# Kernel optimization log

Measured on AMD Instinct MI355X. Metric: run time of the kernel, lower is better.

The kernel has to match this reference:

```python
import jax, jax.numpy as jnp
import numpy as np

N_EMBD = 2048
EXPAND = 2
D_INNER = N_EMBD * EXPAND          # 4096
D_STATE = 128
N_HEADS = D_INNER // D_STATE       # 32
HEAD_DIM = D_INNER // N_HEADS      # 128
N_GROUPS = 1
D_CONV = 4
CHUNK = 64
N_LAYERS = 48
GS = N_GROUPS * D_STATE
PROJ = 2 * D_INNER + N_HEADS + 2 * GS  # 8480
RMS_EPS = 1e-6


def _ssd_scan(A, B, C, dt, x, chunk_size=CHUNK):
    """Mamba-2 SSD chunked selective scan. A:(b,t,h) B,C:(b,t,g,n) dt:(b,t,h) x:(b,t,h,p)."""
    batch, seq_len, n_heads, P = x.shape
    G, N = B.shape[2], B.shape[3]
    Hg = n_heads // G
    Q = chunk_size
    pad_len = -seq_len % Q
    if pad_len:
        A = jnp.pad(A, ((0, 0), (0, pad_len), (0, 0)))
        B = jnp.pad(B, ((0, 0), (0, pad_len), (0, 0), (0, 0)))
        C = jnp.pad(C, ((0, 0), (0, pad_len), (0, 0), (0, 0)))
        dt = jnp.pad(dt, ((0, 0), (0, pad_len), (0, 0)))
        x = jnp.pad(x, ((0, 0), (0, pad_len), (0, 0), (0, 0)))
    T_pad = seq_len + pad_len
    n_chunks = T_pad // Q
    A_c = A.reshape(batch, n_chunks, Q, n_heads)
    B_c = B.reshape(batch, n_chunks, Q, G, N)
    C_c = C.reshape(batch, n_chunks, Q, G, N)
    dt_c = dt.reshape(batch, n_chunks, Q, n_heads)
    x_c = x.reshape(batch, n_chunks, Q, n_heads, P)
    log_a = A_c * dt_c
    cum_log_a = jnp.cumsum(log_a, axis=2)
    chunk_log_decay = cum_log_a[:, :, -1, :]
    log_diff = cum_log_a[:, :, :, None, :] - cum_log_a[:, :, None, :, :]
    causal = jnp.tril(jnp.ones((Q, Q), dtype=jnp.bool_))[None, None, :, :, None]
    L = jnp.exp(jnp.where(causal, log_diff, -jnp.inf))
    CB = jnp.einsum('bcign,bcjgn->bcijg', C_c, B_c)
    L_rs = L.reshape(batch, n_chunks, Q, Q, G, Hg)
    dt_rs = dt_c.reshape(batch, n_chunks, Q, G, Hg)
    x_rs = x_c.reshape(batch, n_chunks, Q, G, Hg, P)
    y_intra = jnp.einsum('bcijGH,bcijG,bcjGH,bcjGHp->bciGHp', L_rs, CB, dt_rs, x_rs)
    decay_to_end = jnp.exp(chunk_log_decay[:, :, None, :] - cum_log_a)
    decay_to_end_rs = decay_to_end.reshape(batch, n_chunks, Q, G, Hg)
    state_local = jnp.einsum('bcjGH,bcjGH,bcjGn,bcjGHp->bcGHnp', decay_to_end_rs, dt_rs, B_c, x_rs)
    chunk_decay = jnp.exp(chunk_log_decay).reshape(batch, n_chunks, G, Hg)

    def scan_op(left, right):
        d_l, s_l = left
        d_r, s_r = right
        return (d_l * d_r, d_r[..., None, None] * s_l + s_r)

    _, state_at_end = jax.lax.associative_scan(scan_op, (chunk_decay, state_local), axis=1)
    state_at_start = jnp.concatenate([jnp.zeros_like(state_at_end[:, :1]), state_at_end[:, :-1]], axis=1)
    decay_from_start = jnp.exp(cum_log_a).reshape(batch, n_chunks, Q, G, Hg)
    y_inter = jnp.einsum('bciGH,bciGn,bcGHnp->bciGHp', decay_from_start, C_c, state_at_start)
    y = (y_intra + y_inter).reshape(batch, T_pad, n_heads, P)
    if pad_len:
        y = y[:, :seq_len]
    return y


def setup_inputs() -> dict:
    key = jax.random.key(0)
    ks = jax.random.split(key, 6)
    Bsz, T = 2, 2048
    x = jax.random.normal(ks[0], (Bsz, T, N_EMBD), jnp.float32)
    norm_scale = jnp.ones((N_EMBD,), jnp.float32)
    in_proj_w = 0.02 * jax.random.normal(ks[1], (N_EMBD, PROJ), jnp.float32)
    conv_weight = 0.02 * jax.random.normal(ks[2], (D_CONV, D_INNER), jnp.float32)
    conv_bias = jnp.zeros((D_INNER,), jnp.float32)
    A_log = jnp.log(jnp.arange(1, N_HEADS + 1, dtype=jnp.float32))
    dt_bias = 0.1 * jax.random.normal(ks[3], (N_HEADS,), jnp.float32)
    D = jnp.ones((D_INNER,), jnp.float32)
    out_proj_w = (0.02 / np.sqrt(2 * N_LAYERS)) * jax.random.normal(ks[4], (D_INNER, N_EMBD), jnp.float32)
    return dict(x=x, norm_scale=norm_scale, in_proj_w=in_proj_w, conv_weight=conv_weight,
                conv_bias=conv_bias, A_log=A_log, dt_bias=dt_bias, D=D, out_proj_w=out_proj_w)


def reference(x, norm_scale, in_proj_w, conv_weight, conv_bias, A_log, dt_bias, D, out_proj_w):
    residual = x
    b, t = x.shape[0], x.shape[1]
    # RMSNorm
    h = x * jax.lax.rsqrt(jnp.mean(x * x, axis=-1, keepdims=True) + RMS_EPS) * norm_scale
    proj = h @ in_proj_w  # (b, t, PROJ)
    gate = proj[..., :D_INNER]
    ssm_in = proj[..., D_INNER:2 * D_INNER]
    dt_raw = proj[..., 2 * D_INNER:2 * D_INNER + N_HEADS]
    Bm = proj[..., 2 * D_INNER + N_HEADS:2 * D_INNER + N_HEADS + GS].reshape(b, t, N_GROUPS, D_STATE)
    Cm = proj[..., 2 * D_INNER + N_HEADS + GS:].reshape(b, t, N_GROUPS, D_STATE)
    # causal depthwise short conv
    xp = jnp.pad(ssm_in, ((0, 0), (D_CONV - 1, 0), (0, 0)))
    w_t = conv_weight.T[:, None, :]  # (D_INNER, 1, D_CONV)
    y = jax.lax.conv_general_dilated(jnp.transpose(xp, (0, 2, 1)), w_t,
                                     window_strides=(1,), padding='VALID',
                                     feature_group_count=D_INNER)
    ssm_in = jnp.transpose(y, (0, 2, 1)) + conv_bias
    ssm_in = jax.nn.silu(ssm_in)
    dt = jax.nn.softplus(dt_raw + dt_bias)
    A = -jnp.exp(A_log)
    A_f = jnp.broadcast_to(A[None, None, :], (b, t, N_HEADS))
    x_h = ssm_in.reshape(b, t, N_HEADS, HEAD_DIM)
    y_ssd = _ssd_scan(A_f, Bm, Cm, dt, x_h).reshape(b, t, D_INNER)
    y_ssd = y_ssd + D * ssm_in
    y_ssd = y_ssd * jax.nn.silu(gate)
    return residual + y_ssd @ out_proj_w
```

## Files before the change

kernel.cpp:

```cpp
#include <hip/hip_runtime.h>

typedef unsigned short u16;
typedef unsigned short u16x8 __attribute__((ext_vector_type(8)));
typedef __bf16 bf16x8 __attribute__((ext_vector_type(8)));
typedef float f32x4 __attribute__((ext_vector_type(4)));


__device__ __forceinline__ float bf2f(u16 u) {
    union { unsigned int i; float f; } v; v.i = ((unsigned int)u) << 16; return v.f;
}
__device__ __forceinline__ u16 f2bf(float f) {
    unsigned int u = __float_as_uint(f);
    u += 0x7fffu + ((u >> 16) & 1u);
    return (u16)(u >> 16);
}
__device__ __forceinline__ bf16x8 ld8(const u16* p) {
    return __builtin_bit_cast(bf16x8, *reinterpret_cast<const u16x8*>(p));
}
__device__ __forceinline__ void load_lds16(const u16* g, u16* l) {
    __builtin_amdgcn_global_load_lds(
        (const __attribute__((address_space(1))) unsigned int*)g,
        (__attribute__((address_space(3))) unsigned int*)l, 16, 0, 0);
}
__device__ __forceinline__ float fexp(float x) { return __expf(x); }
__device__ __forceinline__ float frcp(float x) { return __builtin_amdgcn_rcpf(x); }

__global__ __launch_bounds__(256) void k_rmsnorm(const float* __restrict__ x,
                                                 const float* __restrict__ scale,
                                                 u16* __restrict__ h) {
    int row = blockIdx.x, tid = threadIdx.x;
    const float4* xr = reinterpret_cast<const float4*>(x + (size_t)row * 2048);
    float4 v0 = xr[tid], v1 = xr[tid + 256];
    float ss = v0.x*v0.x + v0.y*v0.y + v0.z*v0.z + v0.w*v0.w
             + v1.x*v1.x + v1.y*v1.y + v1.z*v1.z + v1.w*v1.w;
#pragma unroll
    for (int off = 32; off > 0; off >>= 1) ss += __shfl_down(ss, off, 64);
    __shared__ float red[4];
    if ((tid & 63) == 0) red[tid >> 6] = ss;
    __syncthreads();
    float r = rsqrtf((red[0] + red[1] + red[2] + red[3]) * (1.f / 2048.f) + 1e-6f);
    const float4* sc = reinterpret_cast<const float4*>(scale);
    float4 s0 = sc[tid], s1 = sc[tid + 256];
    ushort4 o0, o1;
    o0.x = f2bf(v0.x * r * s0.x); o0.y = f2bf(v0.y * r * s0.y);
    o0.z = f2bf(v0.z * r * s0.z); o0.w = f2bf(v0.w * r * s0.w);
    o1.x = f2bf(v1.x * r * s1.x); o1.y = f2bf(v1.y * r * s1.y);
    o1.z = f2bf(v1.z * r * s1.z); o1.w = f2bf(v1.w * r * s1.w);
    ushort4* hr = reinterpret_cast<ushort4*>(h + (size_t)row * 2048);
    hr[tid] = o0; hr[tid + 256] = o1;
}

__global__ __launch_bounds__(256) void k_wcast(const float* __restrict__ W,
                                               u16* __restrict__ Wt,
                                               int K, int N) {
    __shared__ u16 Ts[64][72];
    int n0 = blockIdx.x * 64, k0 = blockIdx.y * 64;
    int t = threadIdx.x;
    int jl = (t & 15) * 4;
#pragma unroll
    for (int s = 0; s < 4; ++s) {
        int kl = s * 16 + (t >> 4);
        if (n0 + jl + 4 <= N) {
            float4 v = *reinterpret_cast<const float4*>(W + (size_t)(k0 + kl) * N + n0 + jl);
            Ts[kl][jl] = f2bf(v.x); Ts[kl][jl + 1] = f2bf(v.y);
            Ts[kl][jl + 2] = f2bf(v.z); Ts[kl][jl + 3] = f2bf(v.w);
        } else {
#pragma unroll
            for (int e = 0; e < 4; ++e)
                Ts[kl][jl + e] = (n0 + jl + e < N) ? f2bf(W[(size_t)(k0 + kl) * N + n0 + jl + e]) : (u16)0;
        }
    }
    __syncthreads();
    int nl = t >> 2, kl0 = (t & 3) * 16;
    u16 tmp[16];
#pragma unroll
    for (int e = 0; e < 16; ++e) tmp[e] = Ts[kl0 + e][nl];
    u16* dst = Wt + (size_t)(n0 + nl) * K + k0 + kl0;
    *reinterpret_cast<uint4*>(dst) = *reinterpret_cast<uint4*>(tmp);
    *reinterpret_cast<uint4*>(dst + 8) = *reinterpret_cast<uint4*>(tmp + 8);
}

template <bool BF16_OUT, int MAP>
__global__ __launch_bounds__(256) void k_gemm128(const u16* __restrict__ A,
                                                 const u16* __restrict__ Bt,
                                                 u16* __restrict__ Cb,
                                                 float* __restrict__ Cf,
                                                 const float* __restrict__ resid,
                                                 int M, int Nw, int ldc, int ncoff,
                                                 int K, int nbt) {
    __shared__ u16 As[8192];
    __shared__ u16 Bs[8192];
    int bid = blockIdx.x;
    int mb, nb;
    if (MAP == 0) {
        int mt = M >> 7;
        int grp = mt * 8;
        int g = bid / grp, l = bid % grp;
        nb = g * 8 + (l & 7); mb = l >> 3;
        if (nb * 128 >= Nw) return;
    } else {
        nb = bid % nbt; mb = bid / nbt;
    }
    int m0 = mb * 128, n0 = nb * 128;

    int t = threadIdx.x, lane = t & 63, w = t >> 6;
    int row = t >> 2, kc = (t & 3) * 8;
    int wm = (w >> 1) * 64, wn = (w & 1) * 64;
    int r = lane & 15, q = lane >> 4;

    f32x4 acc[4][4];
#pragma unroll
    for (int a = 0; a < 4; ++a)
#pragma unroll
        for (int b = 0; b < 4; ++b) acc[a][b] = (f32x4){0.f, 0.f, 0.f, 0.f};

    const u16* ga0 = A + (size_t)(m0 + row) * K + kc;
    const u16* ga1 = A + (size_t)(m0 + 64 + row) * K + kc;
    const u16* gb0 = Bt + (size_t)(ncoff + n0 + row) * K + kc;
    const u16* gb1 = Bt + (size_t)(ncoff + n0 + 64 + row) * K + kc;

    for (int k0 = 0; k0 < K; k0 += 64) {
        load_lds16(ga0 + k0,      As + w * 512);
        load_lds16(ga1 + k0,      As + 2048 + w * 512);
        load_lds16(gb0 + k0,      Bs + w * 512);
        load_lds16(gb1 + k0,      Bs + 2048 + w * 512);
        load_lds16(ga0 + k0 + 32, As + 4096 + w * 512);
        load_lds16(ga1 + k0 + 32, As + 4096 + 2048 + w * 512);
        load_lds16(gb0 + k0 + 32, Bs + 4096 + w * 512);
        load_lds16(gb1 + k0 + 32, Bs + 4096 + 2048 + w * 512);
        __syncthreads();
#pragma unroll
        for (int h = 0; h < 2; ++h) {
            bf16x8 af[4], bf[4];
#pragma unroll
            for (int mi = 0; mi < 4; ++mi) af[mi] = ld8(&As[h * 4096 + (wm + mi * 16 + r) * 32 + q * 8]);
#pragma unroll
            for (int ni = 0; ni < 4; ++ni) bf[ni] = ld8(&Bs[h * 4096 + (wn + ni * 16 + r) * 32 + q * 8]);
#pragma unroll
            for (int mi = 0; mi < 4; ++mi)
#pragma unroll
                for (int ni = 0; ni < 4; ++ni)
                    acc[mi][ni] = __builtin_amdgcn_mfma_f32_16x16x32_bf16(af[mi], bf[ni], acc[mi][ni], 0, 0, 0);
        }
        __syncthreads();
    }
#pragma unroll
    for (int mi = 0; mi < 4; ++mi)
#pragma unroll
        for (int ni = 0; ni < 4; ++ni) {
            int lgn = n0 + wn + ni * 16 + r;
            if (lgn < Nw) {
#pragma unroll
                for (int rg = 0; rg < 4; ++rg) {
                    int gm = m0 + wm + mi * 16 + q * 4 + rg;
                    float vv = acc[mi][ni][rg];
                    if (BF16_OUT) {
                        Cb[(size_t)gm * ldc + ncoff + lgn] = f2bf(vv);
                    } else {
                        if (resid) vv += resid[(size_t)gm * ldc + ncoff + lgn];
                        Cf[(size_t)gm * ldc + ncoff + lgn] = vv;
                    }
                }
            }
        }
}

template <bool F32OUT>
__global__ __launch_bounds__(512, 2) void k_gemm256(const u16* __restrict__ A,
                                                    const u16* __restrict__ Bt,
                                                    u16* __restrict__ Cb,
                                                    float* __restrict__ Cf,
                                                    int M, int Nout, int ldc,
                                                    int lda, int Kl) {
    __shared__ u16 lds[65536];
    const int nkt = Kl >> 6;
    int mt = M >> 8;
    int bid = blockIdx.x;
    int swz = (bid & 7) * ((int)gridDim.x >> 3) + (bid >> 3);
    int tiles = mt * (Nout >> 8);
    int tp = swz % tiles, ks = swz / tiles;
    int mb = tp % mt, nb = tp / mt;
    int m0 = mb << 8, n0 = nb << 8;
    int koff = ks * Kl;

    int t = threadIdx.x;
    int ln = t & 63, w = t >> 6;
    int wm = w >> 2, wn = w & 3;
    int r = ln & 15, q = ln >> 4;
    int xq = (q << 3) ^ ((r & 7) << 3);

    int rr = ln >> 3;
    int cc8 = ((ln & 7) ^ rr) << 3;
    const u16* Ag = A + (size_t)(m0 + w * 8 + rr) * lda + koff + cc8;
    const u16* Bg = Bt + (size_t)(n0 + w * 8 + rr) * lda + koff + cc8;
    u16* ldsw = lds + (w << 9);
    const size_t R64 = (size_t)lda * 64;
    const size_t R128 = (size_t)lda * 128;

    f32x4 acc[8][4];
#pragma unroll
    for (int a = 0; a < 8; ++a)
#pragma unroll
        for (int b = 0; b < 4; ++b) acc[a][b] = (f32x4){0.f, 0.f, 0.f, 0.f};

    auto stageA = [&](int ti, int h) {
        if (ti >= nkt) return;
        const u16* g = Ag + ((size_t)ti << 6) + (h ? R128 : (size_t)0);
        u16* d = ldsw + ((ti & 1) << 14) + (h << 13);
        load_lds16(g, d);
        load_lds16(g + R64, d + 4096);
    };
    auto stageB = [&](int ti, int h) {
        if (ti >= nkt) return;
        const u16* g = Bg + ((size_t)ti << 6) + (h ? R128 : (size_t)0);
        u16* d = ldsw + 32768 + ((ti & 1) << 14) + (h << 13);
        load_lds16(g, d);
        load_lds16(g + R64, d + 4096);
    };

    stageA(0, 0); stageA(0, 1); stageB(0, 0); stageB(0, 1);
    stageA(1, 0); stageA(1, 1); stageB(1, 0); stageB(1, 1);
    asm volatile("s_waitcnt vmcnt(8)" ::: "memory");
    __builtin_amdgcn_s_barrier();
    asm volatile("" ::: "memory");

    bf16x8 aF[4][2], bLo[2][2], bHi[2][2];

    for (int kt = 0; kt < nkt; ++kt) {
        const u16* Ah = lds + ((kt & 1) << 14) + (wm << 13);
        const u16* Bh = lds + 32768 + ((kt & 1) << 14) + ((wn >> 1) << 13) + ((wn & 1) << 12);

#pragma unroll
        for (int mi = 0; mi < 4; ++mi)
#pragma unroll
            for (int ks2 = 0; ks2 < 2; ++ks2)
                aF[mi][ks2] = ld8(Ah + (mi * 16 + r) * 64 + (xq ^ (ks2 << 5)));
#pragma unroll
        for (int ni = 0; ni < 2; ++ni)
#pragma unroll
            for (int ks2 = 0; ks2 < 2; ++ks2)
                bLo[ni][ks2] = ld8(Bh + (ni * 16 + r) * 64 + (xq ^ (ks2 << 5)));
        asm volatile("" ::: "memory");
        __builtin_amdgcn_s_barrier();
        asm volatile("s_waitcnt lgkmcnt(0)" ::: "memory");
        __builtin_amdgcn_s_setprio(1);
#pragma unroll
        for (int mi = 0; mi < 4; ++mi)
#pragma unroll
            for (int ni = 0; ni < 2; ++ni)
#pragma unroll
                for (int ks2 = 0; ks2 < 2; ++ks2)
                    acc[mi][ni] = __builtin_amdgcn_mfma_f32_16x16x32_bf16(aF[mi][ks2], bLo[ni][ks2], acc[mi][ni], 0, 0, 0);
        __builtin_amdgcn_s_setprio(0);
        asm volatile("" ::: "memory");
        __builtin_amdgcn_s_barrier();
        asm volatile("" ::: "memory");

#pragma unroll
        for (int ni = 0; ni < 2; ++ni)
#pragma unroll
            for (int ks2 = 0; ks2 < 2; ++ks2)
                bHi[ni][ks2] = ld8(Bh + ((ni + 2) * 16 + r) * 64 + (xq ^ (ks2 << 5)));
        asm volatile("" ::: "memory");
        __builtin_amdgcn_s_barrier();
        asm volatile("s_waitcnt lgkmcnt(0)" ::: "memory");
        __builtin_amdgcn_s_setprio(1);
#pragma unroll
        for (int mi = 0; mi < 4; ++mi)
#pragma unroll
            for (int ni = 0; ni < 2; ++ni)
#pragma unroll
                for (int ks2 = 0; ks2 < 2; ++ks2)
                    acc[mi][ni + 2] = __builtin_amdgcn_mfma_f32_16x16x32_bf16(aF[mi][ks2], bHi[ni][ks2], acc[mi][ni + 2], 0, 0, 0);
        __builtin_amdgcn_s_setprio(0);
        asm volatile("" ::: "memory");
        __builtin_amdgcn_s_barrier();
        asm volatile("" ::: "memory");

#pragma unroll
        for (int mi = 0; mi < 4; ++mi)
#pragma unroll
            for (int ks2 = 0; ks2 < 2; ++ks2)
                aF[mi][ks2] = ld8(Ah + ((mi + 4) * 16 + r) * 64 + (xq ^ (ks2 << 5)));
        stageB(kt + 2, 0);
        stageB(kt + 2, 1);
        asm volatile("" ::: "memory");
        __builtin_amdgcn_s_barrier();
        asm volatile("s_waitcnt lgkmcnt(0)" ::: "memory");
        __builtin_amdgcn_s_setprio(1);
#pragma unroll
        for (int mi = 0; mi < 4; ++mi)
#pragma unroll
            for (int ni = 0; ni < 2; ++ni)
#pragma unroll
                for (int ks2 = 0; ks2 < 2; ++ks2)
                    acc[mi + 4][ni + 2] = __builtin_amdgcn_mfma_f32_16x16x32_bf16(aF[mi][ks2], bHi[ni][ks2], acc[mi + 4][ni + 2], 0, 0, 0);
        __builtin_amdgcn_s_setprio(0);
        asm volatile("" ::: "memory");
        __builtin_amdgcn_s_barrier();
        asm volatile("" ::: "memory");

        stageA(kt + 2, 0);
        stageA(kt + 2, 1);
        __builtin_amdgcn_s_setprio(1);
#pragma unroll
        for (int mi = 0; mi < 4; ++mi)
#pragma unroll
            for (int ni = 0; ni < 2; ++ni)
#pragma unroll
                for (int ks2 = 0; ks2 < 2; ++ks2)
                    acc[mi + 4][ni] = __builtin_amdgcn_mfma_f32_16x16x32_bf16(aF[mi][ks2], bLo[ni][ks2], acc[mi + 4][ni], 0, 0, 0);
        __builtin_amdgcn_s_setprio(0);
        if (kt + 2 < nkt) { asm volatile("s_waitcnt vmcnt(8)" ::: "memory"); }
        else              { asm volatile("s_waitcnt vmcnt(0)" ::: "memory"); }
        __builtin_amdgcn_s_barrier();
        asm volatile("" ::: "memory");
    }

#pragma unroll
    for (int mi = 0; mi < 8; ++mi)
#pragma unroll
        for (int ni = 0; ni < 4; ++ni) {
            int gn = n0 + wn * 64 + ni * 16 + r;
            if (gn < Nout) {
#pragma unroll
                for (int rg = 0; rg < 4; ++rg) {
                    int gm = m0 + wm * 128 + mi * 16 + q * 4 + rg;
                    if (F32OUT) {
                        Cf[(size_t)ks * M * Nout + (size_t)gm * Nout + gn] = acc[mi][ni][rg];
                    } else {
                        Cb[(size_t)gm * ldc + gn] = f2bf(acc[mi][ni][rg]);
                    }
                }
            }
        }
}

__global__ __launch_bounds__(256) void k_addred(const float* __restrict__ x,
                                                const float* __restrict__ P0,
                                                const float* __restrict__ P1,
                                                float* __restrict__ out) {
    const float4* xv = reinterpret_cast<const float4*>(x);
    const float4* a = reinterpret_cast<const float4*>(P0);
    const float4* b = reinterpret_cast<const float4*>(P1);
    float4* o = reinterpret_cast<float4*>(out);
    for (int k = blockIdx.x * 256 + threadIdx.x; k < 2097152; k += 524288) {
        float4 xx = xv[k], aa = a[k], bb = b[k];
        float4 r;
        r.x = xx.x + aa.x + bb.x; r.y = xx.y + aa.y + bb.y;
        r.z = xx.z + aa.z + bb.z; r.w = xx.w + aa.w + bb.w;
        o[k] = r;
    }
}

__global__ __launch_bounds__(64) void k_dt(const u16* __restrict__ proj,
                                           const float* __restrict__ A_log,
                                           const float* __restrict__ dt_bias,
                                           float* __restrict__ dt,
                                           float* __restrict__ cumla) {
    int bid = blockIdx.x;
    int b = bid >> 10, hh = (bid >> 5) & 31, c = bid & 31;
    int j = threadIdx.x;
    int t = c * 64 + j;
    float z = bf2f(proj[(size_t)(b * 2048 + t) * 8480 + 8192 + hh]) + dt_bias[hh];
    float dtv = (z > 20.f) ? z : log1pf(fexp(z));
    float v = -fexp(A_log[hh]) * dtv;
#pragma unroll
    for (int off = 1; off < 64; off <<= 1) {
        float pv = __shfl_up(v, off, 64);
        if (j >= off) v += pv;
    }
    int base = ((b * 32 + hh) * 32 + c) * 64;
    dt[base + j] = dtv;
    cumla[base + j] = v;
}

__global__ __launch_bounds__(256) void k_intra(const u16* __restrict__ proj,
                                               const float* __restrict__ dt,
                                               const float* __restrict__ cumla,
                                               const float* __restrict__ cw,
                                               const float* __restrict__ cb,
                                               const float* __restrict__ Dv,
                                               u16* __restrict__ ybuf,
                                               u16* __restrict__ states) {
    __shared__ u16 Xt[128][72];
    __shared__ u16 Bt[128][72];
    __shared__ union {
        u16 Ms[64][72];
        struct { float cwl[4][128]; float cbl[128]; } cv;
    } sh;
    __shared__ float dts[64], clas[64];
    int bid = blockIdx.x;
    int b = bid >> 10, c = (bid >> 5) & 31, hh = bid & 31;
    int tid = threadIdx.x, lane = tid & 63, w = tid >> 6;
    int r = lane & 15, q = lane >> 4;
    int t0 = b * 2048 + c * 64;
    int sbase = ((b * 32 + hh) * 32 + c) * 64;

    if (tid < 64) { dts[tid] = dt[sbase + tid]; clas[tid] = cumla[sbase + tid]; }
    if (tid < 128) {
        sh.cv.cbl[tid] = cb[hh * 128 + tid];
#pragma unroll
        for (int k = 0; k < 4; ++k) sh.cv.cwl[k][tid] = cw[k * 4096 + hh * 128 + tid];
    }
    __syncthreads();

    {
        int j = tid & 63;
        float wj = fexp(clas[63] - clas[j]) * dts[j];
        for (int g = tid >> 6; g < 16; g += 4) {
            int p0 = g * 8;
            u16 tb[8];
            *reinterpret_cast<uint4*>(tb) =
                *reinterpret_cast<const uint4*>(proj + (size_t)(t0 + j) * 8480 + 8224 + p0);
            float xv[8];
#pragma unroll
            for (int e = 0; e < 8; ++e) xv[e] = sh.cv.cbl[p0 + e];
#pragma unroll
            for (int kk = 0; kk < 4; ++kk) {
                int tl = c * 64 + j - 3 + kk;
                if (tl >= 0) {
                    u16 srow[8];
                    *reinterpret_cast<uint4*>(srow) =
                        *reinterpret_cast<const uint4*>(proj + (size_t)(b * 2048 + tl) * 8480 + 4096 + hh * 128 + p0);
#pragma unroll
                    for (int e = 0; e < 8; ++e) xv[e] += sh.cv.cwl[kk][p0 + e] * bf2f(srow[e]);
                }
            }
#pragma unroll
            for (int e = 0; e < 8; ++e) {
                float s = xv[e] * frcp(1.f + fexp(-xv[e]));
                Xt[p0 + e][j] = f2bf(s);
                Bt[p0 + e][j] = f2bf(wj * bf2f(tb[e]));
            }
        }
    }
    __syncthreads();

    {
        const u16* crow = proj + (size_t)(t0 + w * 16 + r) * 8480 + 8352;
        bf16x8 af[4];
#pragma unroll
        for (int k = 0; k < 4; ++k) af[k] = ld8(crow + k * 32 + q * 8);
#pragma unroll
        for (int tj = 0; tj < 4; ++tj) {
            const u16* brow = proj + (size_t)(t0 + tj * 16 + r) * 8480 + 8224;
            f32x4 acc = (f32x4){0.f, 0.f, 0.f, 0.f};
#pragma unroll
            for (int k = 0; k < 4; ++k)
                acc = __builtin_amdgcn_mfma_f32_16x16x32_bf16(af[k], ld8(brow + k * 32 + q * 8), acc, 0, 0, 0);
            int j = tj * 16 + r;
            float dj = dts[j], cj = clas[j];
#pragma unroll
            for (int rg = 0; rg < 4; ++rg) {
                int i = w * 16 + q * 4 + rg;
                float m = (j <= i) ? acc[rg] * fexp(clas[i] - cj) * dj : 0.f;
                sh.Ms[i][j] = f2bf(m);
            }
        }
    }
    __syncthreads();

    {
        bf16x8 af[2];
#pragma unroll
        for (int k = 0; k < 2; ++k) af[k] = ld8(&sh.Ms[w * 16 + r][k * 32 + q * 8]);
#pragma unroll
        for (int tj = 0; tj < 8; ++tj) {
            f32x4 acc = (f32x4){0.f, 0.f, 0.f, 0.f};
#pragma unroll
            for (int k = 0; k < 2; ++k)
                acc = __builtin_amdgcn_mfma_f32_16x16x32_bf16(af[k], ld8(&Xt[tj * 16 + r][k * 32 + q * 8]), acc, 0, 0, 0);
            int p = tj * 16 + r;
            float dv = Dv[hh * 128 + p];
#pragma unroll
            for (int rg = 0; rg < 4; ++rg) {
                int i = w * 16 + q * 4 + rg;
                float v = acc[rg] + dv * bf2f(Xt[p][i]);
                ybuf[(size_t)(t0 + i) * 4096 + hh * 128 + p] = f2bf(v);
            }
        }
    }

    size_t sb = ((size_t)((b * 32 + hh) * 32 + c)) * 16384;
#pragma unroll
    for (int th = 0; th < 2; ++th) {
        int ti = w + th * 4;
        bf16x8 af[2];
#pragma unroll
        for (int k = 0; k < 2; ++k) af[k] = ld8(&Xt[ti * 16 + r][k * 32 + q * 8]);
#pragma unroll
        for (int tj = 0; tj < 8; ++tj) {
            f32x4 acc = (f32x4){0.f, 0.f, 0.f, 0.f};
#pragma unroll
            for (int k = 0; k < 2; ++k)
                acc = __builtin_amdgcn_mfma_f32_16x16x32_bf16(af[k], ld8(&Bt[tj * 16 + r][k * 32 + q * 8]), acc, 0, 0, 0);
            int n = tj * 16 + r;
#pragma unroll
            for (int rg = 0; rg < 4; ++rg) {
                int p = ti * 16 + q * 4 + rg;
                states[sb + p * 128 + n] = f2bf(acc[rg]);
            }
        }
    }
}

__global__ __launch_bounds__(256) void k_scan(u16* __restrict__ states,
                                              const float* __restrict__ cumla) {
    int gid = blockIdx.x * 256 + threadIdx.x;
    int bh = gid >> 12;
    int q4 = (gid & 4095) * 4;
    size_t base = (size_t)bh * 32 * 16384 + q4;
    float s0 = 0.f, s1 = 0.f, s2 = 0.f, s3 = 0.f;
    for (int c = 0; c < 32; ++c) {
        float cd = fexp(cumla[(bh * 32 + c) * 64 + 63]);
        size_t idx = base + (size_t)c * 16384;
        ushort4 v = *reinterpret_cast<ushort4*>(states + idx);
        float l0 = bf2f(v.x), l1 = bf2f(v.y), l2 = bf2f(v.z), l3 = bf2f(v.w);
        ushort4 o; o.x = f2bf(s0); o.y = f2bf(s1); o.z = f2bf(s2); o.w = f2bf(s3);
        *reinterpret_cast<ushort4*>(states + idx) = o;
        s0 = cd * s0 + l0; s1 = cd * s1 + l1; s2 = cd * s2 + l2; s3 = cd * s3 + l3;
    }
}

__global__ __launch_bounds__(256) void k_inter(const u16* __restrict__ proj,
                                               const u16* __restrict__ states,
                                               const float* __restrict__ cumla,
                                               const u16* __restrict__ ybuf,
                                               u16* __restrict__ ygated) {
    __shared__ u16 Ss[128][136];
    __shared__ float clav[64];
    int bid = blockIdx.x;
    int b = bid >> 10, c = (bid >> 5) & 31, hh = bid & 31;
    int tid = threadIdx.x, lane = tid & 63, w = tid >> 6;
    int r = lane & 15, q = lane >> 4;
    int t0 = b * 2048 + c * 64;
    int sbase = ((b * 32 + hh) * 32 + c) * 64;
    size_t sb = ((size_t)((b * 32 + hh) * 32 + c)) * 16384;

    if (tid < 64) clav[tid] = fexp(cumla[sbase + tid]);
    for (int e = tid; e < 2048; e += 256) {
        int p = e >> 4, n8 = (e & 15) * 8;
        *reinterpret_cast<uint4*>(&Ss[p][n8]) =
            *reinterpret_cast<const uint4*>(states + sb + p * 128 + n8);
    }
    __syncthreads();

    const u16* crow = proj + (size_t)(t0 + w * 16 + r) * 8480 + 8352;
    bf16x8 af[4];
#pragma unroll
    for (int k = 0; k < 4; ++k) af[k] = ld8(crow + k * 32 + q * 8);
#pragma unroll
    for (int tj = 0; tj < 8; ++tj) {
        f32x4 acc = (f32x4){0.f, 0.f, 0.f, 0.f};
#pragma unroll
        for (int k = 0; k < 4; ++k)
            acc = __builtin_amdgcn_mfma_f32_16x16x32_bf16(af[k], ld8(&Ss[tj * 16 + r][k * 32 + q * 8]), acc, 0, 0, 0);
        int p = tj * 16 + r;
        int ch = hh * 128 + p;
#pragma unroll
        for (int rg = 0; rg < 4; ++rg) {
            int i = w * 16 + q * 4 + rg;
            size_t td = (size_t)(t0 + i) * 4096 + ch;
            float v = clav[i] * acc[rg] + bf2f(ybuf[td]);
            float g = bf2f(proj[(size_t)(t0 + i) * 8480 + ch]);
            ygated[td] = f2bf(v * (g * frcp(1.f + fexp(-g))));
        }
    }
}

extern "C" void kernel_launch(void* const* d_in, const int* in_sizes, int n_in,
                              void* d_out, int out_size, void* d_ws, size_t ws_size,
                              hipStream_t stream) {
    const float* x          = (const float*)d_in[0];
    const float* norm_scale = (const float*)d_in[1];
    const float* in_proj_w  = (const float*)d_in[2];
    const float* conv_w     = (const float*)d_in[3];
    const float* conv_b     = (const float*)d_in[4];
    const float* A_log      = (const float*)d_in[5];
    const float* dt_bias    = (const float*)d_in[6];
    const float* Dv         = (const float*)d_in[7];
    const float* out_w      = (const float*)d_in[8];
    float* out = (float*)d_out;

    char* ws = (char*)d_ws;
    u16*   states = (u16*)(ws);
    u16*   h      = (u16*)(ws);
    u16*   wbt    = (u16*)(ws + 16777216);
    float* parts  = (float*)(ws);
    u16*   proj   = (u16*)(ws + 67108864);
    u16*   owt    = (u16*)(ws + 136577024);
    u16*   ybuf   = (u16*)(ws + 170131456);
    float* dt     = (float*)(ws + 203685888);
    float* cumla  = (float*)(ws + 204210176);

    k_rmsnorm<<<4096, 256, 0, stream>>>(x, norm_scale, h);
    k_wcast<<<dim3(136, 32), 256, 0, stream>>>(in_proj_w, wbt, 2048, 8480);
    k_gemm128<true, 1><<<96, 256, 0, stream>>>(h, wbt, proj, nullptr, nullptr,
                                               4096, 288, 8480, 8192, 2048, 3);
    k_gemm256<false><<<512, 512, 0, stream>>>(h, wbt, proj, nullptr,
                                              4096, 8192, 8480, 2048, 2048);
    k_dt<<<2048, 64, 0, stream>>>(proj, A_log, dt_bias, dt, cumla);
    k_intra<<<2048, 256, 0, stream>>>(proj, dt, cumla, conv_w, conv_b, Dv, ybuf, states);
    k_scan<<<1024, 256, 0, stream>>>(states, cumla);
    k_inter<<<2048, 256, 0, stream>>>(proj, states, cumla, ybuf, ybuf);
    k_wcast<<<dim3(32, 64), 256, 0, stream>>>(out_w, owt, 4096, 2048);
    k_gemm256<true><<<256, 512, 0, stream>>>(ybuf, owt, nullptr, parts,
                                             4096, 2048, 2048, 4096, 2048);
    k_addred<<<2048, 256, 0, stream>>>(x, parts, parts + 8388608, out);
}
```

Baseline: 548.0 us.

## Split-K the projection tail GEMM and restagger gemm256 prefetch issue

```diff
diff --git a/kernel.cpp b/kernel.cpp
--- a/kernel.cpp
+++ b/kernel.cpp
@@ -80,28 +80,20 @@
     *reinterpret_cast<uint4*>(dst + 8) = *reinterpret_cast<uint4*>(tmp + 8);
 }
 
-template <bool BF16_OUT, int MAP>
-__global__ __launch_bounds__(256) void k_gemm128(const u16* __restrict__ A,
-                                                 const u16* __restrict__ Bt,
-                                                 u16* __restrict__ Cb,
-                                                 float* __restrict__ Cf,
-                                                 const float* __restrict__ resid,
-                                                 int M, int Nw, int ldc, int ncoff,
-                                                 int K, int nbt) {
+template <int SPLITK>
+__global__ __launch_bounds__(256) void k_tail(const u16* __restrict__ A,
+                                              const u16* __restrict__ Bt,
+                                              float* __restrict__ Pf,
+                                              int M, int ncoff, int lda, int nbt) {
     __shared__ u16 As[8192];
     __shared__ u16 Bs[8192];
+    const int Ks = lda / SPLITK;
     int bid = blockIdx.x;
-    int mb, nb;
-    if (MAP == 0) {
-        int mt = M >> 7;
-        int grp = mt * 8;
-        int g = bid / grp, l = bid % grp;
-        nb = g * 8 + (l & 7); mb = l >> 3;
-        if (nb * 128 >= Nw) return;
-    } else {
-        nb = bid % nbt; mb = bid / nbt;
-    }
+    int nb = bid % nbt;
+    int ksl = (bid / nbt) % SPLITK;
+    int mb = bid / (nbt * SPLITK);
     int m0 = mb * 128, n0 = nb * 128;
+    int koff = ksl * Ks;
 
     int t = threadIdx.x, lane = t & 63, w = t >> 6;
     int row = t >> 2, kc = (t & 3) * 8;
@@ -114,12 +106,12 @@
 #pragma unroll
         for (int b = 0; b < 4; ++b) acc[a][b] = (f32x4){0.f, 0.f, 0.f, 0.f};
 
-    const u16* ga0 = A + (size_t)(m0 + row) * K + kc;
-    const u16* ga1 = A + (size_t)(m0 + 64 + row) * K + kc;
-    const u16* gb0 = Bt + (size_t)(ncoff + n0 + row) * K + kc;
-    const u16* gb1 = Bt + (size_t)(ncoff + n0 + 64 + row) * K + kc;
-
-    for (int k0 = 0; k0 < K; k0 += 64) {
+    const u16* ga0 = A + (size_t)(m0 + row) * lda + koff + kc;
+    const u16* ga1 = A + (size_t)(m0 + 64 + row) * lda + koff + kc;
+    const u16* gb0 = Bt + (size_t)(ncoff + n0 + row) * lda + koff + kc;
+    const u16* gb1 = Bt + (size_t)(ncoff + n0 + 64 + row) * lda + koff + kc;
+
+    for (int k0 = 0; k0 < Ks; k0 += 64) {
         load_lds16(ga0 + k0,      As + w * 512);
         load_lds16(ga1 + k0,      As + 2048 + w * 512);
         load_lds16(gb0 + k0,      Bs + w * 512);
@@ -149,20 +141,27 @@
 #pragma unroll
         for (int ni = 0; ni < 4; ++ni) {
             int lgn = n0 + wn + ni * 16 + r;
-            if (lgn < Nw) {
-#pragma unroll
-                for (int rg = 0; rg < 4; ++rg) {
-                    int gm = m0 + wm + mi * 16 + q * 4 + rg;
-                    float vv = acc[mi][ni][rg];
-                    if (BF16_OUT) {
-                        Cb[(size_t)gm * ldc + ncoff + lgn] = f2bf(vv);
-                    } else {
-                        if (resid) vv += resid[(size_t)gm * ldc + ncoff + lgn];
-                        Cf[(size_t)gm * ldc + ncoff + lgn] = vv;
-                    }
-                }
+#pragma unroll
+            for (int rg = 0; rg < 4; ++rg) {
+                int gm = m0 + wm + mi * 16 + q * 4 + rg;
+                Pf[((size_t)ksl * M + gm) * 384 + lgn] = acc[mi][ni][rg];
             }
         }
+}
+
+__global__ __launch_bounds__(256) void k_tailred(const float* __restrict__ Pf,
+                                                 u16* __restrict__ proj) {
+    int gid = blockIdx.x * 256 + threadIdx.x;
+    int rowi = gid / 72, c4 = (gid % 72) * 4;
+    const float4* P = reinterpret_cast<const float4*>(Pf);
+    int idx = rowi * 96 + (c4 >> 2);
+    float4 s0 = P[idx], s1 = P[393216 + idx], s2 = P[786432 + idx], s3 = P[1179648 + idx];
+    ushort4 o;
+    o.x = f2bf(s0.x + s1.x + s2.x + s3.x);
+    o.y = f2bf(s0.y + s1.y + s2.y + s3.y);
+    o.z = f2bf(s0.z + s1.z + s2.z + s3.z);
+    o.w = f2bf(s0.w + s1.w + s2.w + s3.w);
+    *reinterpret_cast<ushort4*>(proj + (size_t)rowi * 8480 + 8192 + c4) = o;
 }
 
 template <bool F32OUT>
@@ -218,9 +217,9 @@
         load_lds16(g + R64, d + 4096);
     };
 
-    stageA(0, 0); stageA(0, 1); stageB(0, 0); stageB(0, 1);
-    stageA(1, 0); stageA(1, 1); stageB(1, 0); stageB(1, 1);
-    asm volatile("s_waitcnt vmcnt(8)" ::: "memory");
+    stageA(0, 0); stageB(0, 0); stageB(0, 1); stageA(0, 1);
+    stageA(1, 0); stageB(1, 0); stageB(1, 1);
+    asm volatile("s_waitcnt vmcnt(6)" ::: "memory");
     __builtin_amdgcn_s_barrier();
     asm volatile("" ::: "memory");
 
@@ -240,6 +239,7 @@
 #pragma unroll
             for (int ks2 = 0; ks2 < 2; ++ks2)
                 bLo[ni][ks2] = ld8(Bh + (ni * 16 + r) * 64 + (xq ^ (ks2 << 5)));
+        stageA(kt + 1, 1);
         asm volatile("" ::: "memory");
         __builtin_amdgcn_s_barrier();
         asm volatile("s_waitcnt lgkmcnt(0)" ::: "memory");
@@ -283,7 +283,6 @@
             for (int ks2 = 0; ks2 < 2; ++ks2)
                 aF[mi][ks2] = ld8(Ah + ((mi + 4) * 16 + r) * 64 + (xq ^ (ks2 << 5)));
         stageB(kt + 2, 0);
-        stageB(kt + 2, 1);
         asm volatile("" ::: "memory");
         __builtin_amdgcn_s_barrier();
         asm volatile("s_waitcnt lgkmcnt(0)" ::: "memory");
@@ -300,8 +299,10 @@
         __builtin_amdgcn_s_barrier();
         asm volatile("" ::: "memory");
 
+        stageB(kt + 2, 1);
         stageA(kt + 2, 0);
-        stageA(kt + 2, 1);
+        asm volatile("" ::: "memory");
+        __builtin_amdgcn_s_barrier();
         __builtin_amdgcn_s_setprio(1);
 #pragma unroll
         for (int mi = 0; mi < 4; ++mi)
@@ -311,7 +312,7 @@
                 for (int ks2 = 0; ks2 < 2; ++ks2)
                     acc[mi + 4][ni] = __builtin_amdgcn_mfma_f32_16x16x32_bf16(aF[mi][ks2], bLo[ni][ks2], acc[mi + 4][ni], 0, 0, 0);
         __builtin_amdgcn_s_setprio(0);
-        if (kt + 2 < nkt) { asm volatile("s_waitcnt vmcnt(8)" ::: "memory"); }
+        if (kt + 2 < nkt) { asm volatile("s_waitcnt vmcnt(6)" ::: "memory"); }
         else              { asm volatile("s_waitcnt vmcnt(0)" ::: "memory"); }
         __builtin_amdgcn_s_barrier();
         asm volatile("" ::: "memory");
@@ -591,13 +592,14 @@
     u16*   proj   = (u16*)(ws + 67108864);
     u16*   owt    = (u16*)(ws + 136577024);
     u16*   ybuf   = (u16*)(ws + 170131456);
+    float* tailP  = (float*)(ws + 170131456);
     float* dt     = (float*)(ws + 203685888);
     float* cumla  = (float*)(ws + 204210176);
 
     k_rmsnorm<<<4096, 256, 0, stream>>>(x, norm_scale, h);
     k_wcast<<<dim3(136, 32), 256, 0, stream>>>(in_proj_w, wbt, 2048, 8480);
-    k_gemm128<true, 1><<<96, 256, 0, stream>>>(h, wbt, proj, nullptr, nullptr,
-                                               4096, 288, 8480, 8192, 2048, 3);
+    k_tail<4><<<384, 256, 0, stream>>>(h, wbt, tailP, 4096, 8192, 2048, 3);
+    k_tailred<<<1152, 256, 0, stream>>>(tailP, proj);
     k_gemm256<false><<<512, 512, 0, stream>>>(h, wbt, proj, nullptr,
                                               4096, 8192, 8480, 2048, 2048);
     k_dt<<<2048, 64, 0, stream>>>(proj, A_log, dt_bias, dt, cumla);
```

After: 525.3 us. 4.1% less time.
